# Kernel tuning notes

Hardware: AMD Instinct MI355X
Metric: run time of the kernel (lower is better)

## Reference

```python
import jax, jax.numpy as jnp
import numpy as np

N = 512       # building thermal nodes (state dim)
M = 9         # inputs: [Tout(t), Q_1..Q_8]
T = 20000     # RK4 grid points
DT = 30.0     # seconds per step (as in docstring example)
N_DATA = 2000 # outside-temperature breakpoints for interp


def setup_inputs() -> dict:
    key = jax.random.key(0)
    kA, kB, kQ, kT, kiv = jax.random.split(key, 5)
    # Stable continuous-time system: spectral radius ~5e-3 -> |lambda*dt| ~ 0.2
    A = (jax.random.normal(kA, (N, N), jnp.float32) * 1e-4
         - 5e-3 * jnp.eye(N, dtype=jnp.float32))
    B = jax.random.normal(kB, (N, M), jnp.float32) * 1e-3
    Q = jax.random.uniform(kQ, (M - 1,), jnp.float32) * 100.0  # heat gains
    t_eval = jnp.arange(T, dtype=jnp.float32) * DT
    # interp1d replacement: sorted breakpoints + diurnal temperature signal
    Tout_t = jnp.linspace(0.0, T * DT, N_DATA).astype(jnp.float32)
    Tout_v = (15.0 + 10.0 * jnp.sin(2.0 * jnp.pi * Tout_t / 86400.0)
              + jax.random.normal(kT, (N_DATA,), jnp.float32))
    iv = 20.0 + jax.random.normal(kiv, (N,), jnp.float32)
    return {"A": A, "B": B, "Q": Q, "Tout_t": Tout_t, "Tout_v": Tout_v,
            "iv": iv, "t_eval": t_eval}


def reference(A, B, Q, Tout_t, Tout_v, iv, t_eval):
    """RK4 (torchdiffeq 3/8-rule fixed-grid) integration of dx/dt = A@x + B@u(t)."""

    def f(t, x):
        Tout = jnp.interp(t, Tout_t, Tout_v)          # on-device interp1d
        u = jnp.concatenate([Tout[None], Q])          # [M]
        return A @ x + B @ u                          # [N]

    def step(x, td):
        t, dt = td
        k1 = f(t, x)
        k2 = f(t + dt / 3.0, x + dt * k1 / 3.0)
        k3 = f(t + dt * 2.0 / 3.0, x + dt * (k2 - k1 / 3.0))
        k4 = f(t + dt, x + dt * (k1 - k2 + k3))
        x_new = x + dt * (k1 + 3.0 * (k2 + k3) + k4) / 8.0
        return x_new, x_new

    ts = t_eval[:-1]
    dts = jnp.diff(t_eval)
    _, xs = jax.lax.scan(step, iv, (ts, dts))         # [T-1, N]
    return jnp.concatenate([iv[None, :], xs], axis=0)  # [T, N]
```

## Files before the change

### kernel.cpp

```cpp
#include <hip/hip_runtime.h>

#define TT    20000
#define CCH   2500
#define RROWS 2501
#define NDATA 2000
#define MSZ   262144

typedef unsigned short u16;
typedef unsigned int   u32;
using f32x4 = __attribute__((ext_vector_type(4))) float;
using s16x8 = __attribute__((ext_vector_type(8))) short;

static constexpr size_t OFF_HT  = 0;
static constexpr size_t OFF_H2T = (size_t)MSZ;
static constexpr size_t OFF_MP  = 2*(size_t)MSZ;
static constexpr size_t OFF_SQ  = 10*(size_t)MSZ;
static constexpr size_t OFF_VEC = 12*(size_t)MSZ;
static constexpr size_t OFF_FJ  = OFF_VEC + 4096;
static constexpr size_t OFF_AL  = OFF_FJ + 163840;
static constexpr size_t OFF_SA  = OFF_AL + 102400;
static constexpr size_t OFF_SB  = OFF_SA + (size_t)RROWS*512;

#define KTN 18

__device__ __forceinline__ u16 f2bf(float f) {
    u32 u = __float_as_uint(f);
    u += 0x7fff + ((u >> 16) & 1);
    return (u16)(u >> 16);
}

#define MICRO_FMA(a, b) do { \
  acc0.x += (a).x*(b).x; acc0.y += (a).x*(b).y; acc0.z += (a).x*(b).z; acc0.w += (a).x*(b).w; \
  acc1.x += (a).y*(b).x; acc1.y += (a).y*(b).y; acc1.z += (a).y*(b).z; acc1.w += (a).y*(b).w; \
  acc2.x += (a).z*(b).x; acc2.y += (a).z*(b).y; acc2.z += (a).z*(b).z; acc2.w += (a).z*(b).w; \
  acc3.x += (a).w*(b).x; acc3.y += (a).w*(b).y; acc3.z += (a).w*(b).z; acc3.w += (a).w*(b).w; \
} while (0)

#define DECL_GEMM_VARS() \
    int t = threadIdx.x; \
    int tx = t & 15, ty = t >> 4; \
    int ar = t & 63, ak4 = (t >> 6) * 4; \
    int bk = t >> 4, bc4 = (t & 15) * 4; \
    float4 acc0 = {0,0,0,0}, acc1 = {0,0,0,0}, acc2 = {0,0,0,0}, acc3 = {0,0,0,0}; \
    (void)tx; (void)ty; (void)ar; (void)ak4; (void)bk; (void)bc4

#define GEMM_CORE_DB(LOADA, LOADB) \
    { float4 ra = LOADA(0); float4 rbv = LOADB(0); \
    As[0][ak4+0][ar]=ra.x; As[0][ak4+1][ar]=ra.y; As[0][ak4+2][ar]=ra.z; As[0][ak4+3][ar]=ra.w; \
    *(float4*)&Bs[0][bk][bc4] = rbv; \
    for (int kt = 1; kt <= 32; kt++) { \
        __syncthreads(); \
        const int cur = (kt - 1) & 1; \
        if (kt < 32) { ra = LOADA(kt); rbv = LOADB(kt); } \
        _Pragma("unroll") \
        for (int kk = 0; kk < 16; kk++) { \
            float4 a = *(const float4*)&As[cur][kk][ty*4]; \
            float4 b = *(const float4*)&Bs[cur][kk][tx*4]; \
            MICRO_FMA(a, b); \
        } \
        if (kt < 32) { const int nb = kt & 1; \
            As[nb][ak4+0][ar]=ra.x; As[nb][ak4+1][ar]=ra.y; As[nb][ak4+2][ar]=ra.z; As[nb][ak4+3][ar]=ra.w; \
            *(float4*)&Bs[nb][bk][bc4] = rbv; } \
    } }

__device__ __forceinline__ void pow_tile(const float* __restrict__ Ap,
                                         const float* __restrict__ Bp,
                                         float* __restrict__ Zp, int idx) {
    __shared__ float As[2][16][68], Bs[2][16][68];
    DECL_GEMM_VARS();
    int rb = (idx >> 3) * 64, cb = (idx & 7) * 64;
#define LA(kt) (*(const float4*)&Ap[(size_t)(rb+ar)*512 + (kt)*16 + ak4])
#define LB(kt) (*(const float4*)&Bp[(size_t)((kt)*16+bk)*512 + cb + bc4])
    GEMM_CORE_DB(LA, LB)
#undef LA
#undef LB
    size_t zb = (size_t)(rb + ty*4)*512 + cb + tx*4;
    *(float4*)&Zp[zb]        = acc0;
    *(float4*)&Zp[zb + 512]  = acc1;
    *(float4*)&Zp[zb + 1024] = acc2;
    *(float4*)&Zp[zb + 1536] = acc3;
}

__device__ __forceinline__ void matvecT128(const float* __restrict__ MT,
                                           const float* __restrict__ x,
                                           float* __restrict__ y, int rb,
                                           const float* __restrict__ gc,
                                           const float* __restrict__ gu1,
                                           const float* __restrict__ gu2) {
    __shared__ float xs[512];
    __shared__ float red2[2][128];
    int t = threadIdx.x;
    xs[t] = x[t]; xs[t + 256] = x[t + 256];
    __syncthreads();
    int rl = t & 127, h = t >> 7;
    size_t col = (size_t)rb + rl;
    float acc = 0.f;
    int k0 = h << 8;
    #pragma unroll 4
    for (int k = k0; k < k0 + 256; k++) acc += MT[(size_t)k*512 + col] * xs[k];
    red2[h][rl] = acc;
    __syncthreads();
    if (t < 128) {
        float s = red2[0][t] + red2[1][t];
        int r = rb + t;
        if (gc) y[r] = 30.f * (gc[r] + 0.5f*gu1[r] + (1.f/6.f)*gu2[r] + (1.f/24.f)*s);
        else    y[r] = s;
    }
}

__device__ __forceinline__ float interp1(float tt, const float* __restrict__ xp,
                                         const float* __restrict__ fp) {
    if (tt <= xp[0]) return fp[0];
    if (tt >= xp[NDATA-1]) return fp[NDATA-1];
    int lo = 0, hi = NDATA - 1;
    while (hi - lo > 1) { int mid = (lo + hi) >> 1; if (xp[mid] <= tt) lo = mid; else hi = mid; }
    float x0 = xp[lo], x1 = xp[lo+1];
    return fp[lo] + (fp[lo+1] - fp[lo]) * (tt - x0) / (x1 - x0);
}

__global__ __launch_bounds__(256) void k_setup(const float* __restrict__ A,
        const float* __restrict__ B, const float* __restrict__ Q,
        const float* __restrict__ te, const float* __restrict__ Tt,
        const float* __restrict__ Tv, const float* __restrict__ iv,
        float* __restrict__ HT, float* __restrict__ vec, float* __restrict__ AL,
        float* __restrict__ out, float* __restrict__ SA) {
    int bx = blockIdx.x, t = threadIdx.x;
    if (bx < 256) {
        __shared__ float Ts[32][33];
        int tr = bx >> 4, tc = bx & 15;
        int rl = t >> 3, cl4 = (t & 7) * 4;
        float4 a = *(const float4*)&A[(size_t)(tr*32 + rl)*512 + tc*32 + cl4];
        Ts[rl][cl4+0] = 30.f*a.x; Ts[rl][cl4+1] = 30.f*a.y;
        Ts[rl][cl4+2] = 30.f*a.z; Ts[rl][cl4+3] = 30.f*a.w;
        __syncthreads();
        float4 o;
        o.x = Ts[cl4+0][rl]; o.y = Ts[cl4+1][rl]; o.z = Ts[cl4+2][rl]; o.w = Ts[cl4+3][rl];
        *(float4*)&HT[(size_t)(tc*32 + rl)*512 + tr*32 + cl4] = o;
    } else if (bx == 256) {
        for (int i = t; i < 512; i += 256) {
            float v = B[i*9];
            float c = 0.f;
            #pragma unroll
            for (int j = 0; j < 8; j++) c += B[i*9 + 1 + j] * Q[j];
            vec[i] = v;
            vec[2560 + i] = c;
        }
    } else if (bx == 257) {
        for (int i = t; i < 512; i += 256) { out[i] = iv[i]; SA[i] = iv[i]; }
    } else {
        int n = (bx - 258) * 256 + t;
        if (n >= TT) return;
        float* a = AL + (size_t)n * 5;
        if (n == TT - 1) { a[0]=a[1]=a[2]=a[3]=a[4]=0.f; return; }
        float tt = te[n];
        float T1 = interp1(tt, Tt, Tv);
        float T2 = interp1(tt + 10.f, Tt, Tv);
        float T3 = interp1(tt + 20.f, Tt, Tv);
        float T4 = interp1(tt + 30.f, Tt, Tv);
        a[0] = 3.75f * (T1 + 3.f*T2 + 3.f*T3 + T4);
        a[1] = 3.75f * (T1 + 2.f*T2 + T3);
        a[2] = 3.75f * (T1*(1.f/3.f) + T2);
        a[3] = 1.25f * T1;
        a[4] = 1.f;
    }
}

__global__ __launch_bounds__(256) void k_h2kv(const float* __restrict__ HT,
                                              float* __restrict__ H2T,
                                              float* __restrict__ vec) {
    int bx = blockIdx.x;
    if (bx < 64) { pow_tile(HT, HT, H2T, bx); return; }
    int sub = bx - 64, which = sub >> 2, rb = (sub & 3) * 128;
    if (which == 0) matvecT128(HT, vec,        vec + 512,  rb, 0, 0, 0);
    else            matvecT128(HT, vec + 2560, vec + 3072, rb, 0, 0, 0);
}

__global__ __launch_bounds__(256) void k_m1kv(const float* __restrict__ HT,
                                              const float* __restrict__ H2T,
                                              float* __restrict__ M1T,
                                              float* __restrict__ vec) {
    int bx = blockIdx.x;
    if (bx < 64) {
        __shared__ float As[2][16][68], Bs[2][16][68];
        DECL_GEMM_VARS();
        int rb = (bx >> 3) * 64, cb = (bx & 7) * 64;
#define LA(kt) ({ size_t off = (size_t)(rb+ar)*512 + (kt)*16 + ak4; \
        float4 h  = *(const float4*)&HT[off]; \
        float4 h2 = *(const float4*)&H2T[off]; \
        float4 r_; \
        r_.x = h.x*(1.f/6.f) + h2.x*(1.f/24.f); r_.y = h.y*(1.f/6.f) + h2.y*(1.f/24.f); \
        r_.z = h.z*(1.f/6.f) + h2.z*(1.f/24.f); r_.w = h.w*(1.f/6.f) + h2.w*(1.f/24.f); \
        int dd = (rb+ar) - ((kt)*16 + ak4); \
        if (dd >= 0 && dd < 4) (&r_.x)[dd] += 0.5f; \
        r_; })
#define LB(kt) (*(const float4*)&H2T[(size_t)((kt)*16+bk)*512 + cb + bc4])
        GEMM_CORE_DB(LA, LB)
#undef LA
#undef LB
        int col = cb + tx*4;
        #pragma unroll
        for (int i = 0; i < 4; i++) {
            int r = rb + ty*4 + i;
            float4 h = *(const float4*)&HT[(size_t)r*512 + col];
            float4* ac = (i==0) ? &acc0 : (i==1) ? &acc1 : (i==2) ? &acc2 : &acc3;
            ac->x += h.x + (r == col+0 ? 1.f : 0.f);
            ac->y += h.y + (r == col+1 ? 1.f : 0.f);
            ac->z += h.z + (r == col+2 ? 1.f : 0.f);
            ac->w += h.w + (r == col+3 ? 1.f : 0.f);
            *(float4*)&M1T[(size_t)r*512 + col] = *ac;
        }
        return;
    }
    int sub = bx - 64, which = sub >> 2, rb = (sub & 3) * 128;
    if (which == 0) matvecT128(HT, vec + 512,  vec + 1024, rb, 0, 0, 0);
    else            matvecT128(HT, vec + 3072, vec + 3584, rb, 0, 0, 0);
}

__global__ __launch_bounds__(256) void k_m2kv(const float* __restrict__ M1T,
                                              float* __restrict__ M2T,
                                              const float* __restrict__ HT,
                                              float* __restrict__ vec) {
    int bx = blockIdx.x;
    if (bx < 64) { pow_tile(M1T, M1T, M2T, bx); return; }
    int sub = bx - 64, which = sub >> 2, rb = (sub & 3) * 128;
    if (which == 0) matvecT128(HT, vec + 1024, vec + 1536, rb, 0, 0, 0);
    else matvecT128(HT, vec + 3584, vec + 2048, rb,
                    vec + 2560, vec + 3072, vec + 3584);
}

__global__ __launch_bounds__(256) void k_pow(const float* __restrict__ A,
                                             const float* __restrict__ B0,
                                             float* __restrict__ Z0) {
    int sel = blockIdx.x >> 6;
    pow_tile(A, B0 + (size_t)sel*MSZ, Z0 + (size_t)sel*MSZ, blockIdx.x & 63);
}

__global__ __launch_bounds__(256) void k_wgen_sq(const float* __restrict__ vec,
                                                 const float* __restrict__ MP,
                                                 float* __restrict__ FJ,
                                                 const float* __restrict__ P,
                                                 float* __restrict__ Pout) {
    int bx = blockIdx.x;
    if (bx >= 64) { pow_tile(P, P, Pout, bx - 64); return; }
    int d = bx >> 3, cb = (bx & 7) * 64;
    int t = threadIdx.x;
    if (d == 0) {
        for (int idx = t; idx < 320; idx += 256) {
            int r = idx >> 6, c = idx & 63;
            float s = vec[(size_t)r*512 + cb + c];
            #pragma unroll
            for (int i = 0; i < 8; i++)
                FJ[((size_t)i*40 + i*5 + r)*512 + cb + c] = s;
        }
        for (int j = 0; j < 7; j++)
            for (int i = j + 1; i < 8; i++)
                for (int idx = t; idx < 320; idx += 256) {
                    int r = idx >> 6, c = idx & 63;
                    FJ[((size_t)j*40 + i*5 + r)*512 + cb + c] = 0.f;
                }
        return;
    }
    __shared__ float Ws[5][512];
    __shared__ float red4[4][5][64];
    const float* Mj = MP + (size_t)(d - 1)*MSZ;
    for (int e = t; e < 2560; e += 256) Ws[e >> 9][e & 511] = vec[e];
    __syncthreads();
    int col = t & 63, kq = t >> 6, k0 = kq * 128;
    float acc[5] = {0.f, 0.f, 0.f, 0.f, 0.f};
    #pragma unroll 4
    for (int k = k0; k < k0 + 128; k++) {
        float m = Mj[(size_t)k*512 + cb + col];
        acc[0] += Ws[0][k]*m; acc[1] += Ws[1][k]*m; acc[2] += Ws[2][k]*m;
        acc[3] += Ws[3][k]*m; acc[4] += Ws[4][k]*m;
    }
    #pragma unroll
    for (int r = 0; r < 5; r++) red4[kq][r][col] = acc[r];
    __syncthreads();
    for (int idx = t; idx < 320; idx += 256) {
        int r = idx >> 6, c = idx & 63;
        float s = red4[0][r][c] + red4[1][r][c] + red4[2][r][c] + red4[3][r][c];
        for (int i = 0; i + d < 8; i++)
            FJ[((size_t)(i + d)*40 + i*5 + r)*512 + cb + c] = s;
    }
}

__global__ __launch_bounds__(256) void k_e40_sq(const float* __restrict__ AL,
                                                const float* __restrict__ FJ,
                                                float* __restrict__ SA1,
                                                const float* __restrict__ P,
                                                float* __restrict__ Pout) {
    int bx = blockIdx.x;
    if (bx >= 320) { pow_tile(P, P, Pout, bx - 320); return; }
    const float* GT = FJ + (size_t)7*40*512;
    int kb = (bx >> 3) * 64, cb = (bx & 7) * 64;
    __shared__ float Ah[64][41], Bsv[40][68];
    int t = threadIdx.x;
    int tx = t & 15, ty = t >> 4;
    #pragma unroll
    for (int m = 0; m < 10; m++) {
        int e = t + 256*m;
        int row = e / 40, q = e - 40*row;
        float v = 0.f;
        if (kb + row < CCH) v = AL[(size_t)(kb + row)*40 + q];
        Ah[row][q] = v;
        int fq = e >> 6, fc = e & 63;
        Bsv[fq][fc] = GT[(size_t)fq*512 + cb + fc];
    }
    __syncthreads();
    float4 acc0 = {0,0,0,0}, acc1 = {0,0,0,0}, acc2 = {0,0,0,0}, acc3 = {0,0,0,0};
    #pragma unroll 8
    for (int q = 0; q < 40; q++) {
        float4 b = *(const float4*)&Bsv[q][tx*4];
        float a0 = Ah[ty*4+0][q], a1 = Ah[ty*4+1][q];
        float a2 = Ah[ty*4+2][q], a3 = Ah[ty*4+3][q];
        acc0.x += a0*b.x; acc0.y += a0*b.y; acc0.z += a0*b.z; acc0.w += a0*b.w;
        acc1.x += a1*b.x; acc1.y += a1*b.y; acc1.z += a1*b.z; acc1.w += a1*b.w;
        acc2.x += a2*b.x; acc2.y += a2*b.y; acc2.z += a2*b.z; acc2.w += a2*b.w;
        acc3.x += a3*b.x; acc3.y += a3*b.y; acc3.z += a3*b.z; acc3.w += a3*b.w;
    }
    int col = cb + tx*4;
    #pragma unroll
    for (int i = 0; i < 4; i++) {
        int k = kb + ty*4 + i;
        if (k < CCH) {
            float4 a = (i==0) ? acc0 : (i==1) ? acc1 : (i==2) ? acc2 : acc3;
            *(float4*)&SA1[(size_t)k*512 + col] = a;
        }
    }
}

__global__ __launch_bounds__(256) void k_scan_sq(const float* __restrict__ Ain,
                                                 float* __restrict__ Aout,
                                                 const float* __restrict__ QT, int shift,
                                                 const float* __restrict__ P,
                                                 float* __restrict__ Pout) {
    int bx = blockIdx.x;
    if (bx >= 320) { pow_tile(P, P, Pout, bx - 320); return; }
    __shared__ float As[2][16][68], Bs[2][16][68];
    DECL_GEMM_VARS();
    int kb = (bx >> 3) * 64, cb = (bx & 7) * 64;
    int xr = kb + ar - shift;
    bool aval = (xr >= 0) && (kb + ar < RROWS);
#define LA(kt) ({ float4 z = {0,0,0,0}; \
        if (aval) z = *(const float4*)&Ain[(size_t)xr*512 + (kt)*16 + ak4]; z; })
#define LB(kt) (*(const float4*)&QT[(size_t)((kt)*16+bk)*512 + cb + bc4])
    GEMM_CORE_DB(LA, LB)
#undef LA
#undef LB
    int col = cb + tx*4;
    #pragma unroll
    for (int i = 0; i < 4; i++) {
        int krow = kb + ty*4 + i;
        if (krow < RROWS) {
            float4 own = *(const float4*)&Ain[(size_t)krow*512 + col];
            float4 a = (i==0) ? acc0 : (i==1) ? acc1 : (i==2) ? acc2 : acc3;
            float4 res = {own.x + a.x, own.y + a.y, own.z + a.z, own.w + a.w};
            *(float4*)&Aout[(size_t)krow*512 + col] = res;
        }
    }
}

__global__ __launch_bounds__(256) void k_mprepB(const float* __restrict__ MPin,
                                                u16* __restrict__ Mbf2,
                                                const float* __restrict__ FJ) {
    int bx = blockIdx.x;
    int t = threadIdx.x;
    if (bx >= 512) {
        int bx2 = bx - 512;
        int j = bx2 >> 1, half = bx2 & 1;
        int col = half*256 + t;
        u16 arr[64];
        #pragma unroll 8
        for (int q = 0; q < 64; q++) {
            float v = (q < 40) ? FJ[((size_t)j*40 + q)*512 + col] : 0.f;
            arr[q] = f2bf(v);
        }
        #pragma unroll
        for (int qh = 0; qh < 2; qh++) {
            u16* d = Mbf2 + ((size_t)(j*KTN + 16 + qh)*512 + col)*32;
            #pragma unroll
            for (int i = 0; i < 4; i++) {
                int b0 = qh*32 + i*8;
                uint4 P;
                P.x = (u32)arr[b0+0] | ((u32)arr[b0+1] << 16);
                P.y = (u32)arr[b0+2] | ((u32)arr[b0+3] << 16);
                P.z = (u32)arr[b0+4] | ((u32)arr[b0+5] << 16);
                P.w = (u32)arr[b0+6] | ((u32)arr[b0+7] << 16);
                *(uint4*)(d + i*8) = P;
            }
        }
        return;
    }
    int j = bx >> 6, tile = bx & 63;
    int kb = (tile >> 3) * 64, cb = (tile & 7) * 64;
    const float* MT = MPin + (size_t)j * MSZ;
    __shared__ float Ts[64][65];
    int lr = t >> 4, lc = (t & 15) * 4;
    #pragma unroll
    for (int p = 0; p < 4; p++) {
        float4 v = *(const float4*)&MT[(size_t)(kb + p*16 + lr)*512 + cb + lc];
        Ts[p*16+lr][lc+0] = v.x; Ts[p*16+lr][lc+1] = v.y;
        Ts[p*16+lr][lc+2] = v.z; Ts[p*16+lr][lc+3] = v.w;
    }
    __syncthreads();
    int r = t >> 2, c16 = (t & 3) * 16;
    u32 pk[8];
    #pragma unroll
    for (int i = 0; i < 8; i++) {
        u32 a = f2bf(Ts[c16 + 2*i][r]);
        u32 b = f2bf(Ts[c16 + 2*i + 1][r]);
        pk[i] = a | (b << 16);
    }
    int ktg = (kb + c16) >> 5;
    u16* dst = Mbf2 + ((size_t)(j*KTN + ktg)*512 + cb + r)*32 + (c16 & 16);
    *(uint4*)dst       = make_uint4(pk[0], pk[1], pk[2], pk[3]);
    *(uint4*)(dst + 8) = make_uint4(pk[4], pk[5], pk[6], pk[7]);
}

__global__ __launch_bounds__(256) void k_mprepA(const float* __restrict__ SS,
                                                const float* __restrict__ AL,
                                                u16* __restrict__ A2) {
    int g = blockIdx.x * 256 + threadIdx.x;
    if (g >= 2528 * KTN * 2) return;
    int half = g & 1;
    int rk = g >> 1;
    int k = rk % 2528;
    int kt = rk / 2528;
    u16 o[16];
    if (kt < 16) {
        if (k < CCH) {
            const float* src = SS + (size_t)k*512 + kt*32 + half*16;
            #pragma unroll
            for (int i = 0; i < 16; i++) o[i] = f2bf(src[i]);
        } else {
            #pragma unroll
            for (int i = 0; i < 16; i++) o[i] = 0;
        }
    } else {
        int q0 = (kt - 16)*32 + half*16;
        #pragma unroll
        for (int i = 0; i < 16; i++) {
            int q = q0 + i;
            float v = (k < CCH && q < 40) ? AL[(size_t)k*40 + q] : 0.f;
            o[i] = f2bf(v);
        }
    }
    u16* d = A2 + ((size_t)kt*2528 + k)*32 + half*16;
    uint4 P0, P1;
    P0.x = (u32)o[0]  | ((u32)o[1]  << 16); P0.y = (u32)o[2]  | ((u32)o[3]  << 16);
    P0.z = (u32)o[4]  | ((u32)o[5]  << 16); P0.w = (u32)o[6]  | ((u32)o[7]  << 16);
    P1.x = (u32)o[8]  | ((u32)o[9]  << 16); P1.y = (u32)o[10] | ((u32)o[11] << 16);
    P1.z = (u32)o[12] | ((u32)o[13] << 16); P1.w = (u32)o[14] | ((u32)o[15] << 16);
    *(uint4*)d       = P0;
    *(uint4*)(d + 8) = P1;
}

__global__ __launch_bounds__(256, 3) void k_final(const u16* __restrict__ A2,
                                               const u16* __restrict__ Mbf2,
                                               float* __restrict__ out) {
    __shared__ char smem[39168];
    u16* Bsu = (u16*)smem;
    u16* Asu = (u16*)(smem + 36864);
    int t = threadIdx.x;
    int lane = t & 63, w = t >> 6;
    int lo16 = lane & 15, hi = lane >> 4;
    int j = blockIdx.x;
    int kb = blockIdx.y * 32;

    f32x4 acc[2][8];
    #pragma unroll
    for (int m = 0; m < 2; m++)
        #pragma unroll
        for (int n = 0; n < 8; n++) acc[m][n] = 0.f;

    const u16* Bj = Mbf2 + (size_t)j*KTN*16384;
    const u16* Ab = A2 + (size_t)kb*32;

    uint4 pb[8]; uint4 pa;
#define PREFETCH(kt) do { \
    const u16* Bs_ = Bj + (size_t)(kt)*16384; \
    _Pragma("unroll") \
    for (int p = 0; p < 8; p++) \
        pb[p] = *(const uint4*)&Bs_[(w*8 + p)*512 + lane*8]; \
    if (t < 128) pa = *(const uint4*)&Ab[(size_t)(kt)*2528*32 + t*8]; \
} while (0)
#define STORE_LDS() do { \
    _Pragma("unroll") \
    for (int p = 0; p < 8; p++) \
        *(uint4*)&Bsu[((w*8 + p)*16 + (lane>>2))*36 + (lane&3)*8] = pb[p]; \
    if (t < 128) *(uint4*)&Asu[(t>>2)*36 + (t&3)*8] = pa; \
} while (0)

    PREFETCH(0);
    for (int kt = 0; kt < KTN; kt++) {
        __syncthreads();
        STORE_LDS();
        __syncthreads();
        if (kt < KTN-1) PREFETCH(kt + 1);
        __builtin_amdgcn_sched_barrier(0);
        s16x8 fa0 = *(const s16x8*)&Asu[(lo16)*36 + hi*8];
        s16x8 fa1 = *(const s16x8*)&Asu[(16 + lo16)*36 + hi*8];
        #pragma unroll
        for (int n = 0; n < 8; n++) {
            s16x8 fb = *(const s16x8*)&Bsu[((size_t)(w*128 + n*16 + lo16))*36 + hi*8];
            acc[0][n] = __builtin_amdgcn_mfma_f32_16x16x32_bf16(fa0, fb, acc[0][n], 0, 0, 0);
            acc[1][n] = __builtin_amdgcn_mfma_f32_16x16x32_bf16(fa1, fb, acc[1][n], 0, 0, 0);
        }
    }
#undef PREFETCH
#undef STORE_LDS

    float* ldsT = (float*)smem;
    #pragma unroll
    for (int m = 0; m < 2; m++) {
        __syncthreads();
        #pragma unroll
        for (int r = 0; r < 4; r++) {
            int rl = hi*4 + r;
            #pragma unroll
            for (int n = 0; n < 8; n++)
                ldsT[rl*516 + w*128 + n*16 + lo16] = acc[m][n][r];
        }
        __syncthreads();
        #pragma unroll
        for (int p = 0; p < 8; p++) {
            int idx = t + p*256;
            int row = idx >> 7, c4 = idx & 127;
            int k = kb + m*16 + row;
            int n_out = 8*k + j + 1;
            if (k < CCH && n_out < TT)
                *(float4*)&out[(size_t)n_out*512 + c4*4] =
                    *(const float4*)&ldsT[row*516 + c4*4];
        }
    }
}

extern "C" void kernel_launch(void* const* d_in, const int* in_sizes, int n_in,
                              void* d_out, int out_size, void* d_ws, size_t ws_size,
                              hipStream_t stream) {
    const float* A  = (const float*)d_in[0];
    const float* B  = (const float*)d_in[1];
    const float* Q  = (const float*)d_in[2];
    const float* Tt = (const float*)d_in[3];
    const float* Tv = (const float*)d_in[4];
    const float* iv = (const float*)d_in[5];
    const float* te = (const float*)d_in[6];
    float* out = (float*)d_out;
    float* w = (float*)d_ws;

    float* HT  = w + OFF_HT;
    float* H2T = w + OFF_H2T;
    float* MP  = w + OFF_MP;
    float* SQ  = w + OFF_SQ;
    float* vec = w + OFF_VEC;
    float* FJ  = w + OFF_FJ;
    float* AL  = w + OFF_AL;
    float* SA  = w + OFF_SA;
    float* SB  = w + OFF_SB;

    float* M16 = H2T;
    float* M32 = HT;
    float* M64 = SQ;
    float* M8  = MP + 7*(size_t)MSZ;
    u16*   Mbf2 = (u16*)SB;
    u16*   A2   = (u16*)w;

    k_setup<<<337, 256, 0, stream>>>(A, B, Q, te, Tt, Tv, iv, HT, vec, AL, out, SA);
    k_h2kv<<<72, 256, 0, stream>>>(HT, H2T, vec);
    k_m1kv<<<72, 256, 0, stream>>>(HT, H2T, MP, vec);
    k_m2kv<<<72, 256, 0, stream>>>(MP, MP + MSZ, HT, vec);
    k_pow<<<128, 256, 0, stream>>>(MP + MSZ, MP, MP + 2*(size_t)MSZ);
    k_pow<<<256, 256, 0, stream>>>(MP + 3*(size_t)MSZ, MP, MP + 4*(size_t)MSZ);
    k_wgen_sq<<<128, 256, 0, stream>>>(vec, MP, FJ, M8, M16);
    k_e40_sq<<<384, 256, 0, stream>>>(AL, FJ, SA + 512, M16, M32);
    k_scan_sq<<<384, 256, 0, stream>>>(SA, SB, M8,  1, M32, M64);
    k_scan_sq<<<320, 256, 0, stream>>>(SB, SA, M16, 2, nullptr, nullptr);
    k_scan_sq<<<320, 256, 0, stream>>>(SA, SB, M32, 4, nullptr, nullptr);
    k_scan_sq<<<320, 256, 0, stream>>>(SB, SA, M64, 8, nullptr, nullptr);
    k_mprepB<<<528, 256, 0, stream>>>(MP, Mbf2, FJ);
    k_mprepA<<<356, 256, 0, stream>>>(SA, AL, A2);
    k_final<<<dim3(8, 79), 256, 0, stream>>>(A2, Mbf2, out);
}
```

Baseline: 570.4 us.

## Stage final GEMM output in workspace stripes, then interleave into output

The final GEMM now writes each stripe of 625 k-rows into a contiguous workspace buffer rather than scattering rows with stride 8 into the output. A separate k_inter kernel then copies those rows into the interleaved output order. The work is split into four stripes, each with its own GEMM and interleave launch. The aim is more contiguous global writes, at the cost of an extra read and write pass over the output, six more launches, and lower GEMM occupancy (160 blocks per launch).

```diff
diff --git a/kernel.cpp b/kernel.cpp
--- a/kernel.cpp
+++ b/kernel.cpp
@@ -22,6 +22,8 @@
 static constexpr size_t OFF_SB  = OFF_SA + (size_t)RROWS*512;
 
 #define KTN 18
+#define KSTRIPE 625
+static constexpr size_t OFF_OUTK = 729088;
 
 __device__ __forceinline__ u16 f2bf(float f) {
     u32 u = __float_as_uint(f);
@@ -455,9 +457,9 @@
     *(uint4*)(d + 8) = P1;
 }
 
-__global__ __launch_bounds__(256, 3) void k_final(const u16* __restrict__ A2,
+__global__ __launch_bounds__(256, 3) void k_gemm(const u16* __restrict__ A2,
                                                const u16* __restrict__ Mbf2,
-                                               float* __restrict__ out) {
+                                               float* __restrict__ OUTK, int k0) {
     __shared__ char smem[39168];
     u16* Bsu = (u16*)smem;
     u16* Asu = (u16*)(smem + 36864);
@@ -465,7 +467,8 @@
     int lane = t & 63, w = t >> 6;
     int lo16 = lane & 15, hi = lane >> 4;
     int j = blockIdx.x;
-    int kb = blockIdx.y * 32;
+    int kbb = blockIdx.y * 32;
+    int kb = k0 + kbb;
 
     f32x4 acc[2][8];
     #pragma unroll
@@ -526,12 +529,26 @@
         for (int p = 0; p < 8; p++) {
             int idx = t + p*256;
             int row = idx >> 7, c4 = idx & 127;
-            int k = kb + m*16 + row;
-            int n_out = 8*k + j + 1;
-            if (k < CCH && n_out < TT)
-                *(float4*)&out[(size_t)n_out*512 + c4*4] =
+            int kk = kbb + m*16 + row;
+            if (kk < KSTRIPE && (k0 + kk) < CCH)
+                *(float4*)&OUTK[(size_t)(j*KSTRIPE + kk)*512 + c4*4] =
                     *(const float4*)&ldsT[row*516 + c4*4];
         }
+    }
+}
+
+__global__ __launch_bounds__(256) void k_inter(const float* __restrict__ OUTK,
+                                               float* __restrict__ out, int k0) {
+    int rbase = blockIdx.x * 125;
+    int nbase = 8*k0 + 1;
+    for (int i = threadIdx.x; i < 125*128; i += 256) {
+        int row = i >> 7, c4 = i & 127;
+        int n = nbase + rbase + row;
+        if (n >= TT) continue;
+        int g = n - 1;
+        int j = g & 7, kk = (g >> 3) - k0;
+        *(float4*)&out[(size_t)n*512 + c4*4] =
+            *(const float4*)&OUTK[(size_t)(j*KSTRIPE + kk)*512 + c4*4];
     }
 }
 
@@ -564,6 +581,7 @@
     float* M8  = MP + 7*(size_t)MSZ;
     u16*   Mbf2 = (u16*)SB;
     u16*   A2   = (u16*)w;
+    float* OUTK = w + OFF_OUTK;
 
     k_setup<<<337, 256, 0, stream>>>(A, B, Q, te, Tt, Tv, iv, HT, vec, AL, out, SA);
     k_h2kv<<<72, 256, 0, stream>>>(HT, H2T, vec);
@@ -579,5 +597,9 @@
     k_scan_sq<<<320, 256, 0, stream>>>(SB, SA, M64, 8, nullptr, nullptr);
     k_mprepB<<<528, 256, 0, stream>>>(MP, Mbf2, FJ);
     k_mprepA<<<356, 256, 0, stream>>>(SA, AL, A2);
-    k_final<<<dim3(8, 79), 256, 0, stream>>>(A2, Mbf2, out);
-}
+    for (int s = 0; s < 4; s++) {
+        int k0 = s * KSTRIPE;
+        k_gemm<<<dim3(8, 20), 256, 0, stream>>>(A2, Mbf2, OUTK, k0);
+        k_inter<<<40, 256, 0, stream>>>(OUTK, out, k0);
+    }
+}
```

Result: slower. 836.0 us (+46.6%).

## Fuse preprocessing kernels into a persistent megakernel with software grid barriers

Applied to the files above, without the earlier changes.

Replaces fourteen separate preprocessing kernel launches with one persistent 256-block kernel. Each former launch becomes a stage that loops over virtual block indices, and stages are separated by an atomic counter/sense grid barrier placed in workspace and reset by a memset. The aim is to remove per-launch overhead and inter-kernel gaps for these small stages. In exchange, stages with more than 256 blocks run serially over virtual blocks, and the barrier relies on all 256 blocks being co-resident; it also has a bounded spin, so a timeout could break correctness.

```diff
diff --git a/kernel.cpp b/kernel.cpp
--- a/kernel.cpp
+++ b/kernel.cpp
@@ -18,6 +18,7 @@
 static constexpr size_t OFF_VEC = 12*(size_t)MSZ;
 static constexpr size_t OFF_FJ  = OFF_VEC + 4096;
 static constexpr size_t OFF_AL  = OFF_FJ + 163840;
+static constexpr size_t OFF_BAR = OFF_AL + 102000;
 static constexpr size_t OFF_SA  = OFF_AL + 102400;
 static constexpr size_t OFF_SB  = OFF_SA + (size_t)RROWS*512;
 
@@ -27,6 +28,26 @@
     u32 u = __float_as_uint(f);
     u += 0x7fff + ((u >> 16) & 1);
     return (u16)(u >> 16);
+}
+
+__device__ __forceinline__ void gridbar(u32* cnt, u32* sns, int nblk) {
+    __syncthreads();
+    if (threadIdx.x == 0) {
+        u32 s = __hip_atomic_load(sns, __ATOMIC_RELAXED, __HIP_MEMORY_SCOPE_AGENT);
+        u32 arrived = __hip_atomic_fetch_add(cnt, 1u, __ATOMIC_ACQ_REL,
+                                             __HIP_MEMORY_SCOPE_AGENT);
+        if (arrived == (u32)(nblk - 1)) {
+            __hip_atomic_store(cnt, 0u, __ATOMIC_RELAXED, __HIP_MEMORY_SCOPE_AGENT);
+            __hip_atomic_store(sns, s + 1u, __ATOMIC_RELEASE, __HIP_MEMORY_SCOPE_AGENT);
+        } else {
+            for (int it = 0; it < (1 << 18); ++it) {
+                if (__hip_atomic_load(sns, __ATOMIC_ACQUIRE,
+                                      __HIP_MEMORY_SCOPE_AGENT) != s) break;
+                __builtin_amdgcn_s_sleep(8);
+            }
+        }
+    }
+    __syncthreads();
 }
 
 #define MICRO_FMA(a, b) do { \
@@ -118,13 +139,14 @@
     return fp[lo] + (fp[lo+1] - fp[lo]) * (tt - x0) / (x1 - x0);
 }
 
-__global__ __launch_bounds__(256) void k_setup(const float* __restrict__ A,
+
+__device__ void dev_setup(int bx, const float* __restrict__ A,
         const float* __restrict__ B, const float* __restrict__ Q,
         const float* __restrict__ te, const float* __restrict__ Tt,
         const float* __restrict__ Tv, const float* __restrict__ iv,
         float* __restrict__ HT, float* __restrict__ vec, float* __restrict__ AL,
         float* __restrict__ out, float* __restrict__ SA) {
-    int bx = blockIdx.x, t = threadIdx.x;
+    int t = threadIdx.x;
     if (bx < 256) {
         __shared__ float Ts[32][33];
         int tr = bx >> 4, tc = bx & 15;
@@ -165,21 +187,17 @@
     }
 }
 
-__global__ __launch_bounds__(256) void k_h2kv(const float* __restrict__ HT,
-                                              float* __restrict__ H2T,
-                                              float* __restrict__ vec) {
-    int bx = blockIdx.x;
+__device__ void dev_h2kv(int bx, const float* __restrict__ HT,
+                         float* __restrict__ H2T, float* __restrict__ vec) {
     if (bx < 64) { pow_tile(HT, HT, H2T, bx); return; }
     int sub = bx - 64, which = sub >> 2, rb = (sub & 3) * 128;
     if (which == 0) matvecT128(HT, vec,        vec + 512,  rb, 0, 0, 0);
     else            matvecT128(HT, vec + 2560, vec + 3072, rb, 0, 0, 0);
 }
 
-__global__ __launch_bounds__(256) void k_m1kv(const float* __restrict__ HT,
-                                              const float* __restrict__ H2T,
-                                              float* __restrict__ M1T,
-                                              float* __restrict__ vec) {
-    int bx = blockIdx.x;
+__device__ void dev_m1kv(int bx, const float* __restrict__ HT,
+                         const float* __restrict__ H2T,
+                         float* __restrict__ M1T, float* __restrict__ vec) {
     if (bx < 64) {
         __shared__ float As[2][16][68], Bs[2][16][68];
         DECL_GEMM_VARS();
@@ -216,11 +234,9 @@
     else            matvecT128(HT, vec + 3072, vec + 3584, rb, 0, 0, 0);
 }
 
-__global__ __launch_bounds__(256) void k_m2kv(const float* __restrict__ M1T,
-                                              float* __restrict__ M2T,
-                                              const float* __restrict__ HT,
-                                              float* __restrict__ vec) {
-    int bx = blockIdx.x;
+__device__ void dev_m2kv(int bx, const float* __restrict__ M1T,
+                         float* __restrict__ M2T, const float* __restrict__ HT,
+                         float* __restrict__ vec) {
     if (bx < 64) { pow_tile(M1T, M1T, M2T, bx); return; }
     int sub = bx - 64, which = sub >> 2, rb = (sub & 3) * 128;
     if (which == 0) matvecT128(HT, vec + 1024, vec + 1536, rb, 0, 0, 0);
@@ -228,19 +244,15 @@
                     vec + 2560, vec + 3072, vec + 3584);
 }
 
-__global__ __launch_bounds__(256) void k_pow(const float* __restrict__ A,
-                                             const float* __restrict__ B0,
-                                             float* __restrict__ Z0) {
-    int sel = blockIdx.x >> 6;
-    pow_tile(A, B0 + (size_t)sel*MSZ, Z0 + (size_t)sel*MSZ, blockIdx.x & 63);
-}
-
-__global__ __launch_bounds__(256) void k_wgen_sq(const float* __restrict__ vec,
-                                                 const float* __restrict__ MP,
-                                                 float* __restrict__ FJ,
-                                                 const float* __restrict__ P,
-                                                 float* __restrict__ Pout) {
-    int bx = blockIdx.x;
+__device__ void dev_pow(int bx, const float* __restrict__ A,
+                        const float* __restrict__ B0, float* __restrict__ Z0) {
+    int sel = bx >> 6;
+    pow_tile(A, B0 + (size_t)sel*MSZ, Z0 + (size_t)sel*MSZ, bx & 63);
+}
+
+__device__ void dev_wgen(int bx, const float* __restrict__ vec,
+                         const float* __restrict__ MP, float* __restrict__ FJ,
+                         const float* __restrict__ P, float* __restrict__ Pout) {
     if (bx >= 64) { pow_tile(P, P, Pout, bx - 64); return; }
     int d = bx >> 3, cb = (bx & 7) * 64;
     int t = threadIdx.x;
@@ -284,12 +296,9 @@
     }
 }
 
-__global__ __launch_bounds__(256) void k_e40_sq(const float* __restrict__ AL,
-                                                const float* __restrict__ FJ,
-                                                float* __restrict__ SA1,
-                                                const float* __restrict__ P,
-                                                float* __restrict__ Pout) {
-    int bx = blockIdx.x;
+__device__ void dev_e40(int bx, const float* __restrict__ AL,
+                        const float* __restrict__ FJ, float* __restrict__ SA1,
+                        const float* __restrict__ P, float* __restrict__ Pout) {
     if (bx >= 320) { pow_tile(P, P, Pout, bx - 320); return; }
     const float* GT = FJ + (size_t)7*40*512;
     int kb = (bx >> 3) * 64, cb = (bx & 7) * 64;
@@ -329,12 +338,10 @@
     }
 }
 
-__global__ __launch_bounds__(256) void k_scan_sq(const float* __restrict__ Ain,
-                                                 float* __restrict__ Aout,
-                                                 const float* __restrict__ QT, int shift,
-                                                 const float* __restrict__ P,
-                                                 float* __restrict__ Pout) {
-    int bx = blockIdx.x;
+__device__ void dev_scan(int bx, const float* __restrict__ Ain,
+                         float* __restrict__ Aout, const float* __restrict__ QT,
+                         int shift, const float* __restrict__ P,
+                         float* __restrict__ Pout) {
     if (bx >= 320) { pow_tile(P, P, Pout, bx - 320); return; }
     __shared__ float As[2][16][68], Bs[2][16][68];
     DECL_GEMM_VARS();
@@ -360,10 +367,8 @@
     }
 }
 
-__global__ __launch_bounds__(256) void k_mprepB(const float* __restrict__ MPin,
-                                                u16* __restrict__ Mbf2,
-                                                const float* __restrict__ FJ) {
-    int bx = blockIdx.x;
+__device__ void dev_mprepB(int bx, const float* __restrict__ MPin,
+                           u16* __restrict__ Mbf2, const float* __restrict__ FJ) {
     int t = threadIdx.x;
     if (bx >= 512) {
         int bx2 = bx - 512;
@@ -417,10 +422,8 @@
     *(uint4*)(dst + 8) = make_uint4(pk[4], pk[5], pk[6], pk[7]);
 }
 
-__global__ __launch_bounds__(256) void k_mprepA(const float* __restrict__ SS,
-                                                const float* __restrict__ AL,
-                                                u16* __restrict__ A2) {
-    int g = blockIdx.x * 256 + threadIdx.x;
+__device__ void dev_mprepA(int g, const float* __restrict__ SS,
+                           const float* __restrict__ AL, u16* __restrict__ A2) {
     if (g >= 2528 * KTN * 2) return;
     int half = g & 1;
     int rk = g >> 1;
@@ -455,6 +458,52 @@
     *(uint4*)(d + 8) = P1;
 }
 
+__global__ __launch_bounds__(256) void k_mega(
+        const float* __restrict__ A, const float* __restrict__ B,
+        const float* __restrict__ Q, const float* __restrict__ te,
+        const float* __restrict__ Tt, const float* __restrict__ Tv,
+        const float* __restrict__ iv, float* __restrict__ w,
+        float* __restrict__ out) {
+    float* HT  = w + OFF_HT;
+    float* H2T = w + OFF_H2T;
+    float* MP  = w + OFF_MP;
+    float* SQ  = w + OFF_SQ;
+    float* vec = w + OFF_VEC;
+    float* FJ  = w + OFF_FJ;
+    float* AL  = w + OFF_AL;
+    float* SA  = w + OFF_SA;
+    float* SB  = w + OFF_SB;
+    float* M16 = H2T;
+    float* M32 = HT;
+    float* M64 = SQ;
+    float* M8  = MP + 7*(size_t)MSZ;
+    u16*   Mbf2 = (u16*)SB;
+    u16*   A2   = (u16*)w;
+    u32*   bar  = (u32*)(w + OFF_BAR);
+
+    const int bx0 = blockIdx.x;
+#define STAGE(N, ...) \
+    for (int bx = bx0; bx < (N); bx += 256) { __VA_ARGS__; __syncthreads(); } \
+    gridbar(bar, bar + 1, 256);
+
+    STAGE(337, dev_setup(bx, A, B, Q, te, Tt, Tv, iv, HT, vec, AL, out, SA))
+    STAGE(72,  dev_h2kv(bx, HT, H2T, vec))
+    STAGE(72,  dev_m1kv(bx, HT, H2T, MP, vec))
+    STAGE(72,  dev_m2kv(bx, MP, MP + MSZ, HT, vec))
+    STAGE(128, dev_pow(bx, MP + MSZ, MP, MP + 2*(size_t)MSZ))
+    STAGE(256, dev_pow(bx, MP + 3*(size_t)MSZ, MP, MP + 4*(size_t)MSZ))
+    STAGE(128, dev_wgen(bx, vec, MP, FJ, M8, M16))
+    STAGE(384, dev_e40(bx, AL, FJ, SA + 512, M16, M32))
+    STAGE(384, dev_scan(bx, SA, SB, M8, 1, M32, M64))
+    STAGE(320, dev_scan(bx, SB, SA, M16, 2, nullptr, nullptr))
+    STAGE(320, dev_scan(bx, SA, SB, M32, 4, nullptr, nullptr))
+    STAGE(320, dev_scan(bx, SB, SA, M64, 8, nullptr, nullptr))
+    STAGE(528, dev_mprepB(bx, MP, Mbf2, FJ))
+    for (int g = bx0*256 + threadIdx.x; g < 2528*KTN*2; g += 65536)
+        dev_mprepA(g, SA, AL, A2);
+#undef STAGE
+}
+
 __global__ __launch_bounds__(256, 3) void k_final(const u16* __restrict__ A2,
                                                const u16* __restrict__ Mbf2,
                                                float* __restrict__ out) {
@@ -548,36 +597,11 @@
     float* out = (float*)d_out;
     float* w = (float*)d_ws;
 
-    float* HT  = w + OFF_HT;
-    float* H2T = w + OFF_H2T;
-    float* MP  = w + OFF_MP;
-    float* SQ  = w + OFF_SQ;
-    float* vec = w + OFF_VEC;
-    float* FJ  = w + OFF_FJ;
-    float* AL  = w + OFF_AL;
-    float* SA  = w + OFF_SA;
-    float* SB  = w + OFF_SB;
-
-    float* M16 = H2T;
-    float* M32 = HT;
-    float* M64 = SQ;
-    float* M8  = MP + 7*(size_t)MSZ;
-    u16*   Mbf2 = (u16*)SB;
-    u16*   A2   = (u16*)w;
-
-    k_setup<<<337, 256, 0, stream>>>(A, B, Q, te, Tt, Tv, iv, HT, vec, AL, out, SA);
-    k_h2kv<<<72, 256, 0, stream>>>(HT, H2T, vec);
-    k_m1kv<<<72, 256, 0, stream>>>(HT, H2T, MP, vec);
-    k_m2kv<<<72, 256, 0, stream>>>(MP, MP + MSZ, HT, vec);
-    k_pow<<<128, 256, 0, stream>>>(MP + MSZ, MP, MP + 2*(size_t)MSZ);
-    k_pow<<<256, 256, 0, stream>>>(MP + 3*(size_t)MSZ, MP, MP + 4*(size_t)MSZ);
-    k_wgen_sq<<<128, 256, 0, stream>>>(vec, MP, FJ, M8, M16);
-    k_e40_sq<<<384, 256, 0, stream>>>(AL, FJ, SA + 512, M16, M32);
-    k_scan_sq<<<384, 256, 0, stream>>>(SA, SB, M8,  1, M32, M64);
-    k_scan_sq<<<320, 256, 0, stream>>>(SB, SA, M16, 2, nullptr, nullptr);
-    k_scan_sq<<<320, 256, 0, stream>>>(SA, SB, M32, 4, nullptr, nullptr);
-    k_scan_sq<<<320, 256, 0, stream>>>(SB, SA, M64, 8, nullptr, nullptr);
-    k_mprepB<<<528, 256, 0, stream>>>(MP, Mbf2, FJ);
-    k_mprepA<<<356, 256, 0, stream>>>(SA, AL, A2);
+    u16* Mbf2 = (u16*)(w + OFF_SB);
+    u16* A2   = (u16*)w;
+    u32* bar  = (u32*)(w + OFF_BAR);
+
+    hipMemsetAsync(bar, 0, 8, stream);
+    k_mega<<<256, 256, 0, stream>>>(A, B, Q, te, Tt, Tv, iv, w, out);
     k_final<<<dim3(8, 79), 256, 0, stream>>>(A2, Mbf2, out);
 }
```

Result: slower. 1.268 ms (+122.2%).
